# Kernel optimization log

Hardware: AMD Instinct MI355X
Metric: run time of the kernel (lower is better)

Reference implementation:

```python
import jax, jax.numpy as jnp
import numpy as np

N_NODES = 2176
N_IN = 64
N_HID = 2048
N_OUT = 64
NODE_DIM = 64
HEADS = 4


def _build_edge_index():
    hs, os_ = N_IN, N_IN + N_HID
    # input -> hidden block (order: for i: for h)
    s1 = np.repeat(np.arange(0, N_IN), N_HID)
    t1 = np.tile(np.arange(hs, os_), N_IN)
    # hidden -> output block (order: for h: for o)
    s2 = np.repeat(np.arange(hs, os_), N_OUT)
    t2 = np.tile(np.arange(os_, N_NODES), N_HID)
    return jnp.asarray(np.stack([np.concatenate([s1, s2]), np.concatenate([t1, t2])]), dtype=jnp.int32)


def setup_inputs() -> dict:
    key = jax.random.key(0)
    ks = jax.random.split(key, 20)
    D, H = NODE_DIM, HEADS
    edge_index = _build_edge_index()  # [2, E]
    E = edge_index.shape[1]

    def xavier(k, shape):
        fan_in, fan_out = shape[0], shape[1]
        lim = float(np.sqrt(6.0 / (fan_in + fan_out)))
        return jax.random.uniform(k, shape, jnp.float32, -lim, lim)

    return {
        "x_input": jax.random.normal(ks[0], (N_IN,), jnp.float32),
        "node_features": jax.random.normal(ks[1], (N_NODES, D), jnp.float32) * 0.1,
        "edge_weights": jax.random.normal(ks[2], (E, 1), jnp.float32) * 0.1,
        "edge_index": edge_index,
        "wq1": xavier(ks[3], (D, D * H)), "wk1": xavier(ks[4], (D, D * H)),
        "wv1": xavier(ks[5], (D, D * H)), "we1": xavier(ks[6], (1, H)),
        "wo1": xavier(ks[7], (D * H, D)), "bo1": jnp.zeros((D,), jnp.float32),
        "wq2": xavier(ks[8], (D, D * H)), "wk2": xavier(ks[9], (D, D * H)),
        "wv2": xavier(ks[10], (D, D * H)), "we2": xavier(ks[11], (1, H)),
        "wo2": xavier(ks[12], (D * H, D)), "bo2": jnp.zeros((D,), jnp.float32),
        "wproj": xavier(ks[13], (D, 1)), "bproj": jnp.zeros((1,), jnp.float32),
        "num_output_nodes": N_OUT,
    }


def _message_pass(x, edge_index, ew, wq, wk, wv, we, wo, bo):
    # x: [N, D_in]; edge_index: [2, E]; ew: [E, 1]
    src, tgt = edge_index[0], edge_index[1]
    dout = wo.shape[1]
    heads = wq.shape[1] // dout
    q = (x[tgt] @ wq).reshape(-1, heads, dout)  # [E, H, D]
    k = (x[src] @ wk).reshape(-1, heads, dout)
    v = (x[src] @ wv).reshape(-1, heads, dout)
    attn = (q * k).sum(-1) / jnp.sqrt(jnp.float32(dout)) + ew @ we  # [E, H]
    # NOTE: the per-target segment-softmax in the torch source is dead code;
    # the effective math is leaky_relu then a global softmax over edges.
    attn = jax.nn.leaky_relu(attn, negative_slope=0.2)
    attn = jax.nn.softmax(attn, axis=0)
    weighted_v = (attn[:, :, None] * v).reshape(-1, heads * dout)  # [E, H*D]
    out = jax.ops.segment_sum(weighted_v, tgt, num_segments=x.shape[0])  # [N, H*D]
    out = out @ wo + bo
    return out + x  # residual (in_channels == out_channels)


def reference(x_input, node_features, edge_weights, edge_index,
              wq1, wk1, wv1, we1, wo1, bo1,
              wq2, wk2, wv2, we2, wo2, bo2,
              wproj, bproj, num_output_nodes):
    n_in = x_input.shape[0]
    x = node_features.at[:n_in, 0].set(x_input)
    x = jax.nn.relu(_message_pass(x, edge_index, edge_weights, wq1, wk1, wv1, we1, wo1, bo1))
    x = jax.nn.relu(_message_pass(x, edge_index, edge_weights, wq2, wk2, wv2, we2, wo2, bo2))
    out_nodes = x[x.shape[0] - num_output_nodes:]
    output = jax.nn.sigmoid(out_nodes @ wproj + bproj).squeeze()
    return output, x
```

## Files before the change

kernel.cpp:

```cpp
#include <hip/hip_runtime.h>
#include <math.h>

#define E1 131072

template<int AR, int K4>
__device__ __forceinline__ void gemm_nn_lds(const float* __restrict__ A,
                                            const float* __restrict__ B,
                                            float acc[AR][4], int tr, int tc) {
  for (int k4 = 0; k4 < K4; ++k4) {
    float4 b0 = *(const float4*)&B[(k4 * 4 + 0) * 68 + tc * 4];
    float4 b1 = *(const float4*)&B[(k4 * 4 + 1) * 68 + tc * 4];
    float4 b2 = *(const float4*)&B[(k4 * 4 + 2) * 68 + tc * 4];
    float4 b3 = *(const float4*)&B[(k4 * 4 + 3) * 68 + tc * 4];
#pragma unroll
    for (int a = 0; a < AR; ++a) {
      float4 av = *(const float4*)&A[(tr + 16 * a) * 68 + k4 * 4];
      acc[a][0] += av.x * b0.x + av.y * b1.x + av.z * b2.x + av.w * b3.x;
      acc[a][1] += av.x * b0.y + av.y * b1.y + av.z * b2.y + av.w * b3.y;
      acc[a][2] += av.x * b0.z + av.y * b1.z + av.z * b2.z + av.w * b3.z;
      acc[a][3] += av.x * b0.w + av.y * b1.w + av.z * b2.w + av.w * b3.w;
    }
  }
}

template<int AR, int K4>
__device__ __forceinline__ void gemm_nn_g(const float* __restrict__ A,
                                          const float* __restrict__ Bg, int ldb,
                                          float acc[AR][4], int tr, int tc) {
  for (int k4 = 0; k4 < K4; ++k4) {
    float4 b0 = *(const float4*)(Bg + (k4 * 4 + 0) * ldb + tc * 4);
    float4 b1 = *(const float4*)(Bg + (k4 * 4 + 1) * ldb + tc * 4);
    float4 b2 = *(const float4*)(Bg + (k4 * 4 + 2) * ldb + tc * 4);
    float4 b3 = *(const float4*)(Bg + (k4 * 4 + 3) * ldb + tc * 4);
#pragma unroll
    for (int a = 0; a < AR; ++a) {
      float4 av = *(const float4*)&A[(tr + 16 * a) * 68 + k4 * 4];
      acc[a][0] += av.x * b0.x + av.y * b1.x + av.z * b2.x + av.w * b3.x;
      acc[a][1] += av.x * b0.y + av.y * b1.y + av.z * b2.y + av.w * b3.y;
      acc[a][2] += av.x * b0.z + av.y * b1.z + av.z * b2.z + av.w * b3.z;
      acc[a][3] += av.x * b0.w + av.y * b1.w + av.z * b2.w + av.w * b3.w;
    }
  }
}

template<int AR, int BR>
__device__ __forceinline__ void gemm_nt_lds(const float* __restrict__ A,
                                            const float* __restrict__ B,
                                            float acc[AR][BR], int tr, int tc) {
  for (int k4 = 0; k4 < 16; ++k4) {
    float4 av[AR], bv[BR];
#pragma unroll
    for (int a = 0; a < AR; ++a) av[a] = *(const float4*)&A[(tr + 16 * a) * 68 + k4 * 4];
#pragma unroll
    for (int b = 0; b < BR; ++b) bv[b] = *(const float4*)&B[(tc + 16 * b) * 68 + k4 * 4];
#pragma unroll
    for (int a = 0; a < AR; ++a)
#pragma unroll
      for (int b = 0; b < BR; ++b)
        acc[a][b] += av[a].x * bv[b].x + av[a].y * bv[b].y +
                     av[a].z * bv[b].z + av[a].w * bv[b].w;
  }
}

template<int AR>
__device__ __forceinline__ void st_tile(float* __restrict__ C, const float acc[AR][4],
                                        int tr, int tc) {
#pragma unroll
  for (int a = 0; a < AR; ++a)
    *(float4*)&C[(tr + 16 * a) * 68 + tc * 4] =
        make_float4(acc[a][0], acc[a][1], acc[a][2], acc[a][3]);
}

__global__ __launch_bounds__(256) void k_attn1(const float* __restrict__ x,
                                               const float* __restrict__ xinp,
                                               const float* __restrict__ wq1,
                                               const float* __restrict__ wk1,
                                               const float* __restrict__ we1,
                                               const float* __restrict__ ew,
                                               const float* __restrict__ wq2,
                                               const float* __restrict__ wk2,
                                               const float* __restrict__ wv1,
                                               const float* __restrict__ wo1,
                                               const float* __restrict__ wv2,
                                               const float* __restrict__ wo2,
                                               float* __restrict__ AggH,
                                               float* __restrict__ part,
                                               float* __restrict__ bsum,
                                               float* __restrict__ Mb,
                                               float* __restrict__ W2b) {
  __shared__ float S_[17408];
  __shared__ float wred[4];
  const int bid = blockIdx.x, tid = threadIdx.x;
  const bool r1 = bid < 256;
  const int tile = (r1 ? bid : bid - 256) >> 2;
  const int h = bid & 3;
  const int j0 = tile * 32;
  const int tr = tid >> 4, tc = tid & 15;
  const float weh = we1[h];

  if (r1) {
    float* A = S_;
    float* B = S_ + 4352;
    float* C = S_ + 6528;
    float* D = S_ + 10880;
    float* G = S_ + 13056;
    for (int t4 = tid; t4 < 1024; t4 += 256) {
      int r = t4 >> 4, c0 = (t4 & 15) * 4;
      float4 v = *(const float4*)(x + t4 * 4);
      if (c0 == 0) v.x = xinp[r];
      *(float4*)&A[r * 68 + c0] = v;
    }
    for (int t4 = tid; t4 < 512; t4 += 256) {
      int r = t4 >> 4, c0 = (t4 & 15) * 4;
      *(float4*)&B[r * 68 + c0] = *(const float4*)(x + (64 + j0 + r) * 64 + c0);
    }
    for (int t4 = tid; t4 < 512; t4 += 256) {
      int i = t4 >> 3, jl0 = (t4 & 7) * 4;
      *(float4*)&G[i * 68 + jl0] = *(const float4*)(ew + i * 2048 + j0 + jl0);
    }
    __syncthreads();
    {
      float kt[4][4];
#pragma unroll
      for (int a = 0; a < 4; ++a)
#pragma unroll
        for (int q = 0; q < 4; ++q) kt[a][q] = 0.f;
      gemm_nn_g<4, 16>(A, wk1 + h * 64, 256, kt, tr, tc);
      st_tile<4>(C, kt, tr, tc);
      float qt[2][4];
#pragma unroll
      for (int a = 0; a < 2; ++a)
#pragma unroll
        for (int q = 0; q < 4; ++q) qt[a][q] = 0.f;
      gemm_nn_g<2, 16>(B, wq1 + h * 64, 256, qt, tr, tc);
      st_tile<2>(D, qt, tr, tc);
    }
    __syncthreads();
    float lg[2][4];
#pragma unroll
    for (int a = 0; a < 2; ++a)
#pragma unroll
      for (int b = 0; b < 4; ++b) lg[a][b] = 0.f;
    gemm_nt_lds<2, 4>(D, C, lg, tr, tc);
    float esum = 0.f;
#pragma unroll
    for (int a = 0; a < 2; ++a) {
      int row = tr + 16 * a;
#pragma unroll
      for (int b = 0; b < 4; ++b) {
        int col = tc + 16 * b;
        float v = lg[a][b] * 0.125f + G[col * 68 + row] * weh;
        v = (v >= 0.f) ? v : 0.2f * v;
        v = fminf(v, 60.f);
        float e = __expf(v);
        esum += e;
        B[row * 68 + col] = e;
      }
    }
#pragma unroll
    for (int s = 1; s < 64; s <<= 1) esum += __shfl_xor(esum, s);
    if ((tid & 63) == 0) wred[tid >> 6] = esum;
    __syncthreads();
    float u[2][4];
#pragma unroll
    for (int a = 0; a < 2; ++a)
#pragma unroll
      for (int q = 0; q < 4; ++q) u[a][q] = 0.f;
    gemm_nn_lds<2, 16>(B, A, u, tr, tc);
#pragma unroll
    for (int a = 0; a < 2; ++a)
      *(float4*)&AggH[(j0 + tr + 16 * a) * 256 + h * 64 + tc * 4] =
          make_float4(u[a][0], u[a][1], u[a][2], u[a][3]);
    if (tid == 0) bsum[bid] = (wred[0] + wred[1]) + (wred[2] + wred[3]);

    if (bid < 12) {
      __syncthreads();
      const int type = bid >> 2, hh = bid & 3;
      if (type == 0) {
        for (int t4 = tid; t4 < 1024; t4 += 256) {
          int k = t4 >> 4, c0 = (t4 & 15) * 4;
          *(float4*)&A[k * 68 + c0] = *(const float4*)(wq2 + k * 256 + hh * 64 + c0);
          *(float4*)&C[k * 68 + c0] = *(const float4*)(wk2 + k * 256 + hh * 64 + c0);
        }
        __syncthreads();
        float m[4][4];
#pragma unroll
        for (int a = 0; a < 4; ++a)
#pragma unroll
          for (int b = 0; b < 4; ++b) m[a][b] = 0.f;
        gemm_nt_lds<4, 4>(A, C, m, tr, tc);
#pragma unroll
        for (int a = 0; a < 4; ++a)
#pragma unroll
          for (int b = 0; b < 4; ++b)
            Mb[hh * 4096 + (tr + 16 * a) * 64 + tc + 16 * b] = m[a][b];
      } else {
        const float* wv = (type == 1) ? wv1 : wv2;
        const float* wo = (type == 1) ? wo1 : wo2;
        for (int t4 = tid; t4 < 1024; t4 += 256) {
          int k = t4 >> 4, c0 = (t4 & 15) * 4;
          *(float4*)&A[k * 68 + c0] = *(const float4*)(wv + k * 256 + hh * 64 + c0);
          *(float4*)&C[k * 68 + c0] = *(const float4*)(wo + (hh * 64 + k) * 64 + c0);
        }
        __syncthreads();
        float m[4][4];
#pragma unroll
        for (int a = 0; a < 4; ++a)
#pragma unroll
          for (int q = 0; q < 4; ++q) m[a][q] = 0.f;
        gemm_nn_lds<4, 16>(A, C, m, tr, tc);
        float* o = W2b + (type - 1) * 16384;
#pragma unroll
        for (int a = 0; a < 4; ++a)
          *(float4*)&o[(hh * 64 + tr + 16 * a) * 64 + tc * 4] =
              make_float4(m[a][0], m[a][1], m[a][2], m[a][3]);
      }
    }
  } else {
    float* A = S_;
    float* B = S_ + 2176;
    float* C = S_ + 6528;
    float* D = S_ + 8704;
    float* G = S_ + 13056;
    for (int t4 = tid; t4 < 512; t4 += 256) {
      int r = t4 >> 4, c0 = (t4 & 15) * 4;
      *(float4*)&A[r * 68 + c0] = *(const float4*)(x + (64 + j0 + r) * 64 + c0);
    }
    for (int t4 = tid; t4 < 1024; t4 += 256) {
      int r = t4 >> 4, c0 = (t4 & 15) * 4;
      *(float4*)&B[r * 68 + c0] = *(const float4*)(x + (2112 + r) * 64 + c0);
    }
    for (int t4 = tid; t4 < 512; t4 += 256) {
      int jl = t4 >> 4, o0 = (t4 & 15) * 4;
      *(float4*)&G[jl * 68 + o0] = *(const float4*)(ew + E1 + (j0 + jl) * 64 + o0);
    }
    __syncthreads();
    {
      float kt[2][4];
#pragma unroll
      for (int a = 0; a < 2; ++a)
#pragma unroll
        for (int q = 0; q < 4; ++q) kt[a][q] = 0.f;
      gemm_nn_g<2, 16>(A, wk1 + h * 64, 256, kt, tr, tc);
      st_tile<2>(C, kt, tr, tc);
      float qt[4][4];
#pragma unroll
      for (int a = 0; a < 4; ++a)
#pragma unroll
        for (int q = 0; q < 4; ++q) qt[a][q] = 0.f;
      gemm_nn_g<4, 16>(B, wq1 + h * 64, 256, qt, tr, tc);
      st_tile<4>(D, qt, tr, tc);
    }
    __syncthreads();
    float lg[4][2];
#pragma unroll
    for (int a = 0; a < 4; ++a)
#pragma unroll
      for (int b = 0; b < 2; ++b) lg[a][b] = 0.f;
    gemm_nt_lds<4, 2>(D, C, lg, tr, tc);
    float esum = 0.f;
#pragma unroll
    for (int a = 0; a < 4; ++a) {
      int row = tr + 16 * a;
#pragma unroll
      for (int b = 0; b < 2; ++b) {
        int col = tc + 16 * b;
        float v = lg[a][b] * 0.125f + G[col * 68 + row] * weh;
        v = (v >= 0.f) ? v : 0.2f * v;
        v = fminf(v, 60.f);
        float e = __expf(v);
        esum += e;
        B[row * 68 + col] = e;
      }
    }
#pragma unroll
    for (int s = 1; s < 64; s <<= 1) esum += __shfl_xor(esum, s);
    if ((tid & 63) == 0) wred[tid >> 6] = esum;
    __syncthreads();
    float u[4][4];
#pragma unroll
    for (int a = 0; a < 4; ++a)
#pragma unroll
      for (int q = 0; q < 4; ++q) u[a][q] = 0.f;
    gemm_nn_lds<4, 8>(B, A, u, tr, tc);
#pragma unroll
    for (int a = 0; a < 4; ++a)
      *(float4*)&part[tile * 16384 + (tr + 16 * a) * 256 + h * 64 + tc * 4] =
          make_float4(u[a][0], u[a][1], u[a][2], u[a][3]);
    if (tid == 0) bsum[bid] = (wred[0] + wred[1]) + (wred[2] + wred[3]);
  }
}

__global__ __launch_bounds__(256) void k_attn2(const float* __restrict__ x,
                                               const float* __restrict__ Mb,
                                               const float* __restrict__ we,
                                               const float* __restrict__ ew,
                                               float* __restrict__ AggH,
                                               float* __restrict__ part,
                                               float* __restrict__ bsum) {
  __shared__ float S_[13056];
  __shared__ float wred[4];
  const int bid = blockIdx.x, tid = threadIdx.x;
  const bool r1 = bid < 256;
  const int tile = (r1 ? bid : bid - 256) >> 2;
  const int h = bid & 3;
  const int j0 = tile * 32;
  const int tr = tid >> 4, tc = tid & 15;
  const float weh = we[h];
  const float* Mh = Mb + h * 4096;

  if (r1) {
    float* A = S_;
    float* B = S_ + 4352;
    float* C = S_ + 6528;
    float* G = S_ + 8704;
    for (int t4 = tid; t4 < 1024; t4 += 256) {
      int r = t4 >> 4, c0 = (t4 & 15) * 4;
      *(float4*)&A[r * 68 + c0] = *(const float4*)(x + t4 * 4);
    }
    for (int t4 = tid; t4 < 512; t4 += 256) {
      int r = t4 >> 4, c0 = (t4 & 15) * 4;
      *(float4*)&B[r * 68 + c0] = *(const float4*)(x + (64 + j0 + r) * 64 + c0);
    }
    for (int t4 = tid; t4 < 512; t4 += 256) {
      int i = t4 >> 3, jl0 = (t4 & 7) * 4;
      *(float4*)&G[i * 68 + jl0] = *(const float4*)(ew + i * 2048 + j0 + jl0);
    }
    __syncthreads();
    {
      float t_[2][4];
#pragma unroll
      for (int a = 0; a < 2; ++a)
#pragma unroll
        for (int q = 0; q < 4; ++q) t_[a][q] = 0.f;
      gemm_nn_g<2, 16>(B, Mh, 64, t_, tr, tc);
      st_tile<2>(C, t_, tr, tc);
    }
    __syncthreads();
    float lg[2][4];
#pragma unroll
    for (int a = 0; a < 2; ++a)
#pragma unroll
      for (int b = 0; b < 4; ++b) lg[a][b] = 0.f;
    gemm_nt_lds<2, 4>(C, A, lg, tr, tc);
    float esum = 0.f;
#pragma unroll
    for (int a = 0; a < 2; ++a) {
      int row = tr + 16 * a;
#pragma unroll
      for (int b = 0; b < 4; ++b) {
        int col = tc + 16 * b;
        float v = lg[a][b] * 0.125f + G[col * 68 + row] * weh;
        v = (v >= 0.f) ? v : 0.2f * v;
        v = fminf(v, 60.f);
        float e = __expf(v);
        esum += e;
        B[row * 68 + col] = e;
      }
    }
#pragma unroll
    for (int s = 1; s < 64; s <<= 1) esum += __shfl_xor(esum, s);
    if ((tid & 63) == 0) wred[tid >> 6] = esum;
    __syncthreads();
    float u[2][4];
#pragma unroll
    for (int a = 0; a < 2; ++a)
#pragma unroll
      for (int q = 0; q < 4; ++q) u[a][q] = 0.f;
    gemm_nn_lds<2, 16>(B, A, u, tr, tc);
#pragma unroll
    for (int a = 0; a < 2; ++a)
      *(float4*)&AggH[(j0 + tr + 16 * a) * 256 + h * 64 + tc * 4] =
          make_float4(u[a][0], u[a][1], u[a][2], u[a][3]);
    if (tid == 0) bsum[bid] = (wred[0] + wred[1]) + (wred[2] + wred[3]);
  } else {
    float* A = S_;
    float* B = S_ + 2176;
    float* C = S_ + 6528;
    float* G = S_ + 10880;
    for (int t4 = tid; t4 < 512; t4 += 256) {
      int r = t4 >> 4, c0 = (t4 & 15) * 4;
      *(float4*)&A[r * 68 + c0] = *(const float4*)(x + (64 + j0 + r) * 64 + c0);
    }
    for (int t4 = tid; t4 < 1024; t4 += 256) {
      int r = t4 >> 4, c0 = (t4 & 15) * 4;
      *(float4*)&B[r * 68 + c0] = *(const float4*)(x + (2112 + r) * 64 + c0);
    }
    for (int t4 = tid; t4 < 512; t4 += 256) {
      int jl = t4 >> 4, o0 = (t4 & 15) * 4;
      *(float4*)&G[jl * 68 + o0] = *(const float4*)(ew + E1 + (j0 + jl) * 64 + o0);
    }
    __syncthreads();
    {
      float t_[4][4];
#pragma unroll
      for (int a = 0; a < 4; ++a)
#pragma unroll
        for (int q = 0; q < 4; ++q) t_[a][q] = 0.f;
      gemm_nn_g<4, 16>(B, Mh, 64, t_, tr, tc);
      st_tile<4>(C, t_, tr, tc);
    }
    __syncthreads();
    float lg[4][2];
#pragma unroll
    for (int a = 0; a < 4; ++a)
#pragma unroll
      for (int b = 0; b < 2; ++b) lg[a][b] = 0.f;
    gemm_nt_lds<4, 2>(C, A, lg, tr, tc);
    float esum = 0.f;
#pragma unroll
    for (int a = 0; a < 4; ++a) {
      int row = tr + 16 * a;
#pragma unroll
      for (int b = 0; b < 2; ++b) {
        int col = tc + 16 * b;
        float v = lg[a][b] * 0.125f + G[col * 68 + row] * weh;
        v = (v >= 0.f) ? v : 0.2f * v;
        v = fminf(v, 60.f);
        float e = __expf(v);
        esum += e;
        B[row * 68 + col] = e;
      }
    }
#pragma unroll
    for (int s = 1; s < 64; s <<= 1) esum += __shfl_xor(esum, s);
    if ((tid & 63) == 0) wred[tid >> 6] = esum;
    __syncthreads();
    float u[4][4];
#pragma unroll
    for (int a = 0; a < 4; ++a)
#pragma unroll
      for (int q = 0; q < 4; ++q) u[a][q] = 0.f;
    gemm_nn_lds<4, 8>(B, A, u, tr, tc);
#pragma unroll
    for (int a = 0; a < 4; ++a)
      *(float4*)&part[tile * 16384 + (tr + 16 * a) * 256 + h * 64 + tc * 4] =
          make_float4(u[a][0], u[a][1], u[a][2], u[a][3]);
    if (tid == 0) bsum[bid] = (wred[0] + wred[1]) + (wred[2] + wred[3]);
  }
}

template<bool SUB, bool HEAD>
__global__ __launch_bounds__(256) void k_proj(const float* __restrict__ xin,
                                              const float* __restrict__ xinp,
                                              const float* __restrict__ AggH,
                                              const float* __restrict__ part,
                                              const float* __restrict__ bsum,
                                              const float* __restrict__ W2,
                                              const float* __restrict__ bo,
                                              const float* __restrict__ wproj,
                                              const float* __restrict__ bproj,
                                              float* __restrict__ xout,
                                              float* __restrict__ outh) {
  __shared__ float As[4][260];
  const int bid = blockIdx.x, tid = threadIdx.x;
  const int n0 = bid * 4;
  const int nl = tid >> 6, d = tid & 63;
  const int node = n0 + nl;

  float inv[4];
  {
    int l = tid & 63;
#pragma unroll
    for (int hh = 0; hh < 4; ++hh) {
      float s = bsum[4 * l + hh] + bsum[256 + 4 * l + hh];
#pragma unroll
      for (int st = 1; st < 64; st <<= 1) s += __shfl_xor(s, st);
      inv[hh] = 1.f / s;
    }
  }

  float xres = xin[node * 64 + d];
  if (SUB) {
    if (d == 0 && node < 64) xres = xinp[node];
  }

  float val;
  if (n0 < 64) {
    val = xres + bo[d];
  } else {
    if (n0 < 2112) {
      int a = tid >> 6, c0 = (tid & 63) * 4;
      float4 v = *(const float4*)&AggH[(n0 - 64 + a) * 256 + c0];
      float iv = inv[c0 >> 6];
      *(float4*)&As[a][c0] = make_float4(v.x * iv, v.y * iv, v.z * iv, v.w * iv);
    } else {
      int a = tid >> 6, c0 = (tid & 63) * 4;
      float4 s = make_float4(0.f, 0.f, 0.f, 0.f);
      for (int ch = 0; ch < 64; ++ch) {
        float4 v = *(const float4*)&part[ch * 16384 + (n0 - 2112 + a) * 256 + c0];
        s.x += v.x; s.y += v.y; s.z += v.z; s.w += v.w;
      }
      float iv = inv[c0 >> 6];
      *(float4*)&As[a][c0] = make_float4(s.x * iv, s.y * iv, s.z * iv, s.w * iv);
    }
    __syncthreads();
    float acc = xres + bo[d];
    for (int c4 = 0; c4 < 64; ++c4) {
      float4 a4 = *(const float4*)&As[nl][c4 * 4];
      acc += a4.x * W2[(c4 * 4 + 0) * 64 + d] + a4.y * W2[(c4 * 4 + 1) * 64 + d] +
             a4.z * W2[(c4 * 4 + 2) * 64 + d] + a4.w * W2[(c4 * 4 + 3) * 64 + d];
    }
    val = acc;
  }
  val = fmaxf(val, 0.f);
  xout[node * 64 + d] = val;

  if (HEAD) {
    if (n0 >= 2112) {
      float wv = val * wproj[d];
#pragma unroll
      for (int st = 1; st < 64; st <<= 1) wv += __shfl_xor(wv, st);
      if ((tid & 63) == 0) outh[node - 2112] = 1.f / (1.f + __expf(-(wv + bproj[0])));
    }
  }
}

extern "C" void kernel_launch(void* const* d_in, const int* in_sizes, int n_in,
                              void* d_out, int out_size, void* d_ws, size_t ws_size,
                              hipStream_t stream) {
  const float* x_input       = (const float*)d_in[0];
  const float* node_features = (const float*)d_in[1];
  const float* edge_weights  = (const float*)d_in[2];
  const float* wq1 = (const float*)d_in[4];
  const float* wk1 = (const float*)d_in[5];
  const float* wv1 = (const float*)d_in[6];
  const float* we1 = (const float*)d_in[7];
  const float* wo1 = (const float*)d_in[8];
  const float* bo1 = (const float*)d_in[9];
  const float* wq2 = (const float*)d_in[10];
  const float* wk2 = (const float*)d_in[11];
  const float* wv2 = (const float*)d_in[12];
  const float* we2 = (const float*)d_in[13];
  const float* wo2 = (const float*)d_in[14];
  const float* bo2 = (const float*)d_in[15];
  const float* wproj = (const float*)d_in[16];
  const float* bproj = (const float*)d_in[17];

  float* out = (float*)d_out;
  float* ws = (float*)d_ws;
  float* xB   = ws;
  float* AggH = xB + 139264;
  float* part = AggH + 524288;
  float* bsum = part + 1048576;
  float* Mb   = bsum + 512;
  float* W2b  = Mb + 16384;

  k_attn1<<<512, 256, 0, stream>>>(node_features, x_input, wq1, wk1, we1, edge_weights,
                                   wq2, wk2, wv1, wo1, wv2, wo2,
                                   AggH, part, bsum, Mb, W2b);
  k_proj<true, false><<<544, 256, 0, stream>>>(node_features, x_input, AggH, part, bsum,
                                               W2b, bo1, nullptr, nullptr, xB, nullptr);
  k_attn2<<<512, 256, 0, stream>>>(xB, Mb, we2, edge_weights, AggH, part, bsum);
  k_proj<false, true><<<544, 256, 0, stream>>>(xB, nullptr, AggH, part, bsum,
                                               W2b + 16384, bo2, wproj, bproj, out + 64, out);
}
```

Measured before the change: 63.60 us.

## Precompute per-head bilinear attention matrices in a prologue kernel

```diff
diff --git a/kernel.cpp b/kernel.cpp
--- a/kernel.cpp
+++ b/kernel.cpp
@@ -4,9 +4,9 @@
 #define E1 131072
 
 template<int AR, int K4>
-__device__ __forceinline__ void gemm_nn_lds(const float* __restrict__ A,
-                                            const float* __restrict__ B,
-                                            float acc[AR][4], int tr, int tc) {
+__device__ __forceinline__ void gemm_nn(const float* __restrict__ A,
+                                        const float* __restrict__ B,
+                                        float acc[AR][4], int tr, int tc) {
   for (int k4 = 0; k4 < K4; ++k4) {
     float4 b0 = *(const float4*)&B[(k4 * 4 + 0) * 68 + tc * 4];
     float4 b1 = *(const float4*)&B[(k4 * 4 + 1) * 68 + tc * 4];
@@ -23,30 +23,10 @@
   }
 }
 
-template<int AR, int K4>
-__device__ __forceinline__ void gemm_nn_g(const float* __restrict__ A,
-                                          const float* __restrict__ Bg, int ldb,
-                                          float acc[AR][4], int tr, int tc) {
-  for (int k4 = 0; k4 < K4; ++k4) {
-    float4 b0 = *(const float4*)(Bg + (k4 * 4 + 0) * ldb + tc * 4);
-    float4 b1 = *(const float4*)(Bg + (k4 * 4 + 1) * ldb + tc * 4);
-    float4 b2 = *(const float4*)(Bg + (k4 * 4 + 2) * ldb + tc * 4);
-    float4 b3 = *(const float4*)(Bg + (k4 * 4 + 3) * ldb + tc * 4);
-#pragma unroll
-    for (int a = 0; a < AR; ++a) {
-      float4 av = *(const float4*)&A[(tr + 16 * a) * 68 + k4 * 4];
-      acc[a][0] += av.x * b0.x + av.y * b1.x + av.z * b2.x + av.w * b3.x;
-      acc[a][1] += av.x * b0.y + av.y * b1.y + av.z * b2.y + av.w * b3.y;
-      acc[a][2] += av.x * b0.z + av.y * b1.z + av.z * b2.z + av.w * b3.z;
-      acc[a][3] += av.x * b0.w + av.y * b1.w + av.z * b2.w + av.w * b3.w;
-    }
-  }
-}
-
 template<int AR, int BR>
-__device__ __forceinline__ void gemm_nt_lds(const float* __restrict__ A,
-                                            const float* __restrict__ B,
-                                            float acc[AR][BR], int tr, int tc) {
+__device__ __forceinline__ void gemm_nt(const float* __restrict__ A,
+                                        const float* __restrict__ B,
+                                        float acc[AR][BR], int tr, int tc) {
   for (int k4 = 0; k4 < 16; ++k4) {
     float4 av[AR], bv[BR];
 #pragma unroll
@@ -71,69 +51,155 @@
         make_float4(acc[a][0], acc[a][1], acc[a][2], acc[a][3]);
 }
 
+__device__ __forceinline__ void ld64(float* __restrict__ dst, const float* __restrict__ src,
+                                     int tid, bool sub, const float* __restrict__ xinp) {
+  for (int t4 = tid; t4 < 1024; t4 += 256) {
+    int r = t4 >> 4, c0 = (t4 & 15) * 4;
+    float4 v = *(const float4*)(src + t4 * 4);
+    if (sub && c0 == 0) v.x = xinp[r];
+    *(float4*)&dst[r * 68 + c0] = v;
+  }
+}
+__device__ __forceinline__ void ld32(float* __restrict__ dst, const float* __restrict__ src,
+                                     int tid) {
+  for (int t4 = tid; t4 < 512; t4 += 256) {
+    int r = t4 >> 4, c0 = (t4 & 15) * 4;
+    *(float4*)&dst[r * 68 + c0] = *(const float4*)(src + t4 * 4);
+  }
+}
+__device__ __forceinline__ void ldw(float* __restrict__ dst, const float* __restrict__ w,
+                                    int h, int tid) {
+  for (int t4 = tid; t4 < 1024; t4 += 256) {
+    int k = t4 >> 4, c0 = (t4 & 15) * 4;
+    *(float4*)&dst[k * 68 + c0] = *(const float4*)(w + k * 256 + h * 64 + c0);
+  }
+}
+
+__global__ __launch_bounds__(256) void k_pre(const float* __restrict__ nf,
+                                             const float* __restrict__ xinp,
+                                             const float* __restrict__ wq1, const float* __restrict__ wk1,
+                                             const float* __restrict__ wv1, const float* __restrict__ wo1,
+                                             const float* __restrict__ bo1,
+                                             const float* __restrict__ wq2, const float* __restrict__ wk2,
+                                             const float* __restrict__ wv2, const float* __restrict__ wo2,
+                                             float* __restrict__ Y1b, float* __restrict__ Y2b,
+                                             float* __restrict__ Y1pb, float* __restrict__ M2b,
+                                             float* __restrict__ W2b) {
+  __shared__ float A[4352];
+  __shared__ float B[4352];
+  __shared__ float C[4352];
+  const int bid = blockIdx.x, tid = threadIdx.x;
+  const int type = bid >> 2, h = bid & 3;
+  const int tr = tid >> 4, tc = tid & 15;
+
+  if (type <= 2) {
+    if (type == 0) {
+      ld64(A, nf, tid, true, xinp);
+    } else if (type == 1) {
+      ld64(A, nf + 2112 * 64, tid, false, nullptr);
+    } else {
+      for (int t4 = tid; t4 < 1024; t4 += 256) {
+        int r = t4 >> 4, c0 = (t4 & 15) * 4;
+        float4 v = *(const float4*)(nf + t4 * 4);
+        if (c0 == 0) v.x = xinp[r];
+        float4 bv = *(const float4*)(bo1 + c0);
+        v.x = fmaxf(v.x + bv.x, 0.f); v.y = fmaxf(v.y + bv.y, 0.f);
+        v.z = fmaxf(v.z + bv.z, 0.f); v.w = fmaxf(v.w + bv.w, 0.f);
+        *(float4*)&A[r * 68 + c0] = v;
+      }
+    }
+    const float* w1 = (type == 0) ? wk1 : (type == 1) ? wq1 : wk2;
+    const float* w2 = (type == 0) ? wq1 : (type == 1) ? wk1 : wq2;
+    ldw(B, w1, h, tid);
+    __syncthreads();
+    float t_[4][4];
+#pragma unroll
+    for (int a = 0; a < 4; ++a)
+#pragma unroll
+      for (int q = 0; q < 4; ++q) t_[a][q] = 0.f;
+    gemm_nn<4, 16>(A, B, t_, tr, tc);
+    __syncthreads();
+    st_tile<4>(C, t_, tr, tc);
+    ldw(B, w2, h, tid);
+    __syncthreads();
+    float y[4][4];
+#pragma unroll
+    for (int a = 0; a < 4; ++a)
+#pragma unroll
+      for (int b = 0; b < 4; ++b) y[a][b] = 0.f;
+    gemm_nt<4, 4>(C, B, y, tr, tc);
+    float* dst = (type == 0) ? Y1b : (type == 1) ? Y2b : Y1pb;
+#pragma unroll
+    for (int a = 0; a < 4; ++a)
+#pragma unroll
+      for (int b = 0; b < 4; ++b)
+        dst[h * 4096 + (tr + 16 * a) * 64 + tc + 16 * b] = y[a][b];
+  } else if (type == 3) {
+    ldw(A, wq2, h, tid);
+    ldw(B, wk2, h, tid);
+    __syncthreads();
+    float m[4][4];
+#pragma unroll
+    for (int a = 0; a < 4; ++a)
+#pragma unroll
+      for (int b = 0; b < 4; ++b) m[a][b] = 0.f;
+    gemm_nt<4, 4>(A, B, m, tr, tc);
+#pragma unroll
+    for (int a = 0; a < 4; ++a)
+#pragma unroll
+      for (int b = 0; b < 4; ++b)
+        M2b[h * 4096 + (tr + 16 * a) * 64 + tc + 16 * b] = m[a][b];
+  } else {
+    const float* wv = (type == 4) ? wv1 : wv2;
+    const float* wo = (type == 4) ? wo1 : wo2;
+    ldw(A, wv, h, tid);
+    for (int t4 = tid; t4 < 1024; t4 += 256) {
+      int t = t4 >> 4, c0 = (t4 & 15) * 4;
+      *(float4*)&B[t * 68 + c0] = *(const float4*)(wo + (h * 64 + t) * 64 + c0);
+    }
+    __syncthreads();
+    float m[4][4];
+#pragma unroll
+    for (int a = 0; a < 4; ++a)
+#pragma unroll
+      for (int q = 0; q < 4; ++q) m[a][q] = 0.f;
+    gemm_nn<4, 16>(A, B, m, tr, tc);
+    float* o = W2b + (type - 4) * 16384;
+#pragma unroll
+    for (int a = 0; a < 4; ++a)
+      *(float4*)&o[(h * 64 + tr + 16 * a) * 64 + tc * 4] =
+          make_float4(m[a][0], m[a][1], m[a][2], m[a][3]);
+  }
+}
+
 __global__ __launch_bounds__(256) void k_attn1(const float* __restrict__ x,
                                                const float* __restrict__ xinp,
-                                               const float* __restrict__ wq1,
-                                               const float* __restrict__ wk1,
-                                               const float* __restrict__ we1,
+                                               const float* __restrict__ Y1b,
+                                               const float* __restrict__ Y2b,
+                                               const float* __restrict__ we,
                                                const float* __restrict__ ew,
-                                               const float* __restrict__ wq2,
-                                               const float* __restrict__ wk2,
-                                               const float* __restrict__ wv1,
-                                               const float* __restrict__ wo1,
-                                               const float* __restrict__ wv2,
-                                               const float* __restrict__ wo2,
                                                float* __restrict__ AggH,
                                                float* __restrict__ part,
-                                               float* __restrict__ bsum,
-                                               float* __restrict__ Mb,
-                                               float* __restrict__ W2b) {
-  __shared__ float S_[17408];
+                                               float* __restrict__ bsum) {
+  __shared__ float S_[13184];
   __shared__ float wred[4];
   const int bid = blockIdx.x, tid = threadIdx.x;
-  const bool r1 = bid < 256;
-  const int tile = (r1 ? bid : bid - 256) >> 2;
   const int h = bid & 3;
-  const int j0 = tile * 32;
   const int tr = tid >> 4, tc = tid & 15;
-  const float weh = we1[h];
-
-  if (r1) {
-    float* A = S_;
-    float* B = S_ + 4352;
-    float* C = S_ + 6528;
-    float* D = S_ + 10880;
-    float* G = S_ + 13056;
-    for (int t4 = tid; t4 < 1024; t4 += 256) {
-      int r = t4 >> 4, c0 = (t4 & 15) * 4;
-      float4 v = *(const float4*)(x + t4 * 4);
-      if (c0 == 0) v.x = xinp[r];
-      *(float4*)&A[r * 68 + c0] = v;
-    }
-    for (int t4 = tid; t4 < 512; t4 += 256) {
-      int r = t4 >> 4, c0 = (t4 & 15) * 4;
-      *(float4*)&B[r * 68 + c0] = *(const float4*)(x + (64 + j0 + r) * 64 + c0);
-    }
+  const float weh = we[h];
+
+  if (bid < 256) {
+    const int j0 = (bid >> 2) * 32;
+    float* XS = S_;
+    float* Y  = S_ + 4352;
+    float* XH = S_ + 8704;
+    float* G  = S_ + 10880;
+    ld64(XS, x, tid, true, xinp);
+    ld64(Y, Y1b + h * 4096, tid, false, nullptr);
+    ld32(XH, x + (64 + j0) * 64, tid);
     for (int t4 = tid; t4 < 512; t4 += 256) {
       int i = t4 >> 3, jl0 = (t4 & 7) * 4;
-      *(float4*)&G[i * 68 + jl0] = *(const float4*)(ew + i * 2048 + j0 + jl0);
-    }
-    __syncthreads();
-    {
-      float kt[4][4];
-#pragma unroll
-      for (int a = 0; a < 4; ++a)
-#pragma unroll
-        for (int q = 0; q < 4; ++q) kt[a][q] = 0.f;
-      gemm_nn_g<4, 16>(A, wk1 + h * 64, 256, kt, tr, tc);
-      st_tile<4>(C, kt, tr, tc);
-      float qt[2][4];
-#pragma unroll
-      for (int a = 0; a < 2; ++a)
-#pragma unroll
-        for (int q = 0; q < 4; ++q) qt[a][q] = 0.f;
-      gemm_nn_g<2, 16>(B, wq1 + h * 64, 256, qt, tr, tc);
-      st_tile<2>(D, qt, tr, tc);
+      *(float4*)&G[i * 36 + jl0] = *(const float4*)(ew + i * 2048 + j0 + jl0);
     }
     __syncthreads();
     float lg[2][4];
@@ -141,123 +207,199 @@
     for (int a = 0; a < 2; ++a)
 #pragma unroll
       for (int b = 0; b < 4; ++b) lg[a][b] = 0.f;
-    gemm_nt_lds<2, 4>(D, C, lg, tr, tc);
-    float esum = 0.f;
+    gemm_nt<2, 4>(XH, Y, lg, tr, tc);
+    float e_[2][4], esum = 0.f;
 #pragma unroll
     for (int a = 0; a < 2; ++a) {
       int row = tr + 16 * a;
 #pragma unroll
       for (int b = 0; b < 4; ++b) {
+        int col = tc + 16 * b;
+        float v = lg[a][b] * 0.125f + G[col * 36 + row] * weh;
+        v = (v >= 0.f) ? v : 0.2f * v;
+        v = fminf(v, 60.f);
+        float e = __expf(v);
+        e_[a][b] = e; esum += e;
+      }
+    }
+#pragma unroll
+    for (int s = 1; s < 64; s <<= 1) esum += __shfl_xor(esum, s);
+    if ((tid & 63) == 0) wred[tid >> 6] = esum;
+    __syncthreads();
+#pragma unroll
+    for (int a = 0; a < 2; ++a)
+#pragma unroll
+      for (int b = 0; b < 4; ++b)
+        XH[(tr + 16 * a) * 68 + tc + 16 * b] = e_[a][b];
+    __syncthreads();
+    float u[2][4];
+#pragma unroll
+    for (int a = 0; a < 2; ++a)
+#pragma unroll
+      for (int q = 0; q < 4; ++q) u[a][q] = 0.f;
+    gemm_nn<2, 16>(XH, XS, u, tr, tc);
+#pragma unroll
+    for (int a = 0; a < 2; ++a)
+      *(float4*)&AggH[(j0 + tr + 16 * a) * 256 + h * 64 + tc * 4] =
+          make_float4(u[a][0], u[a][1], u[a][2], u[a][3]);
+    if (tid == 0) bsum[bid] = (wred[0] + wred[1]) + (wred[2] + wred[3]);
+  } else {
+    const int tile = (bid - 256) >> 2;
+    const int j0 = tile * 32;
+    float* Y  = S_;
+    float* XH = S_ + 4352;
+    float* G  = S_ + 6528;
+    ld64(Y, Y2b + h * 4096, tid, false, nullptr);
+    ld32(XH, x + (64 + j0) * 64, tid);
+    for (int t4 = tid; t4 < 512; t4 += 256) {
+      int jl = t4 >> 4, o0 = (t4 & 15) * 4;
+      *(float4*)&G[jl * 68 + o0] = *(const float4*)(ew + E1 + (j0 + jl) * 64 + o0);
+    }
+    __syncthreads();
+    float lg[4][2];
+#pragma unroll
+    for (int a = 0; a < 4; ++a)
+#pragma unroll
+      for (int b = 0; b < 2; ++b) lg[a][b] = 0.f;
+    gemm_nt<4, 2>(Y, XH, lg, tr, tc);
+    float e_[4][2], esum = 0.f;
+#pragma unroll
+    for (int a = 0; a < 4; ++a) {
+      int row = tr + 16 * a;
+#pragma unroll
+      for (int b = 0; b < 2; ++b) {
         int col = tc + 16 * b;
         float v = lg[a][b] * 0.125f + G[col * 68 + row] * weh;
         v = (v >= 0.f) ? v : 0.2f * v;
         v = fminf(v, 60.f);
         float e = __expf(v);
-        esum += e;
-        B[row * 68 + col] = e;
+        e_[a][b] = e; esum += e;
       }
     }
 #pragma unroll
     for (int s = 1; s < 64; s <<= 1) esum += __shfl_xor(esum, s);
     if ((tid & 63) == 0) wred[tid >> 6] = esum;
     __syncthreads();
+#pragma unroll
+    for (int a = 0; a < 4; ++a)
+#pragma unroll
+      for (int b = 0; b < 2; ++b)
+        Y[(tr + 16 * a) * 68 + tc + 16 * b] = e_[a][b];
+    __syncthreads();
+    float u[4][4];
+#pragma unroll
+    for (int a = 0; a < 4; ++a)
+#pragma unroll
+      for (int q = 0; q < 4; ++q) u[a][q] = 0.f;
+    gemm_nn<4, 8>(Y, XH, u, tr, tc);
+#pragma unroll
+    for (int a = 0; a < 4; ++a)
+      *(float4*)&part[tile * 16384 + (tr + 16 * a) * 256 + h * 64 + tc * 4] =
+          make_float4(u[a][0], u[a][1], u[a][2], u[a][3]);
+    if (tid == 0) bsum[bid] = (wred[0] + wred[1]) + (wred[2] + wred[3]);
+  }
+}
+
+__global__ __launch_bounds__(256) void k_attn2(const float* __restrict__ x,
+                                               const float* __restrict__ Y1pb,
+                                               const float* __restrict__ M2b,
+                                               const float* __restrict__ we,
+                                               const float* __restrict__ ew,
+                                               float* __restrict__ AggH,
+                                               float* __restrict__ part,
+                                               float* __restrict__ bsum) {
+  __shared__ float S_[13184];
+  __shared__ float wred[4];
+  const int bid = blockIdx.x, tid = threadIdx.x;
+  const int h = bid & 3;
+  const int tr = tid >> 4, tc = tid & 15;
+  const float weh = we[h];
+
+  if (bid < 256) {
+    const int j0 = (bid >> 2) * 32;
+    float* XS = S_;
+    float* Y  = S_ + 4352;
+    float* XH = S_ + 8704;
+    float* G  = S_ + 10880;
+    ld64(XS, x, tid, false, nullptr);
+    ld64(Y, Y1pb + h * 4096, tid, false, nullptr);
+    ld32(XH, x + (64 + j0) * 64, tid);
+    for (int t4 = tid; t4 < 512; t4 += 256) {
+      int i = t4 >> 3, jl0 = (t4 & 7) * 4;
+      *(float4*)&G[i * 36 + jl0] = *(const float4*)(ew + i * 2048 + j0 + jl0);
+    }
+    __syncthreads();
+    float lg[2][4];
+#pragma unroll
+    for (int a = 0; a < 2; ++a)
+#pragma unroll
+      for (int b = 0; b < 4; ++b) lg[a][b] = 0.f;
+    gemm_nt<2, 4>(XH, Y, lg, tr, tc);
+    float e_[2][4], esum = 0.f;
+#pragma unroll
+    for (int a = 0; a < 2; ++a) {
+      int row = tr + 16 * a;
+#pragma unroll
+      for (int b = 0; b < 4; ++b) {
+        int col = tc + 16 * b;
+        float v = lg[a][b] * 0.125f + G[col * 36 + row] * weh;
+        v = (v >= 0.f) ? v : 0.2f * v;
+        v = fminf(v, 60.f);
+        float e = __expf(v);
+        e_[a][b] = e; esum += e;
+      }
+    }
+#pragma unroll
+    for (int s = 1; s < 64; s <<= 1) esum += __shfl_xor(esum, s);
+    if ((tid & 63) == 0) wred[tid >> 6] = esum;
+    __syncthreads();
+#pragma unroll
+    for (int a = 0; a < 2; ++a)
+#pragma unroll
+      for (int b = 0; b < 4; ++b)
+        XH[(tr + 16 * a) * 68 + tc + 16 * b] = e_[a][b];
+    __syncthreads();
     float u[2][4];
 #pragma unroll
     for (int a = 0; a < 2; ++a)
 #pragma unroll
       for (int q = 0; q < 4; ++q) u[a][q] = 0.f;
-    gemm_nn_lds<2, 16>(B, A, u, tr, tc);
+    gemm_nn<2, 16>(XH, XS, u, tr, tc);
 #pragma unroll
     for (int a = 0; a < 2; ++a)
       *(float4*)&AggH[(j0 + tr + 16 * a) * 256 + h * 64 + tc * 4] =
           make_float4(u[a][0], u[a][1], u[a][2], u[a][3]);
     if (tid == 0) bsum[bid] = (wred[0] + wred[1]) + (wred[2] + wred[3]);
-
-    if (bid < 12) {
-      __syncthreads();
-      const int type = bid >> 2, hh = bid & 3;
-      if (type == 0) {
-        for (int t4 = tid; t4 < 1024; t4 += 256) {
-          int k = t4 >> 4, c0 = (t4 & 15) * 4;
-          *(float4*)&A[k * 68 + c0] = *(const float4*)(wq2 + k * 256 + hh * 64 + c0);
-          *(float4*)&C[k * 68 + c0] = *(const float4*)(wk2 + k * 256 + hh * 64 + c0);
-        }
-        __syncthreads();
-        float m[4][4];
-#pragma unroll
-        for (int a = 0; a < 4; ++a)
-#pragma unroll
-          for (int b = 0; b < 4; ++b) m[a][b] = 0.f;
-        gemm_nt_lds<4, 4>(A, C, m, tr, tc);
-#pragma unroll
-        for (int a = 0; a < 4; ++a)
-#pragma unroll
-          for (int b = 0; b < 4; ++b)
-            Mb[hh * 4096 + (tr + 16 * a) * 64 + tc + 16 * b] = m[a][b];
-      } else {
-        const float* wv = (type == 1) ? wv1 : wv2;
-        const float* wo = (type == 1) ? wo1 : wo2;
-        for (int t4 = tid; t4 < 1024; t4 += 256) {
-          int k = t4 >> 4, c0 = (t4 & 15) * 4;
-          *(float4*)&A[k * 68 + c0] = *(const float4*)(wv + k * 256 + hh * 64 + c0);
-          *(float4*)&C[k * 68 + c0] = *(const float4*)(wo + (hh * 64 + k) * 64 + c0);
-        }
-        __syncthreads();
-        float m[4][4];
-#pragma unroll
-        for (int a = 0; a < 4; ++a)
-#pragma unroll
-          for (int q = 0; q < 4; ++q) m[a][q] = 0.f;
-        gemm_nn_lds<4, 16>(A, C, m, tr, tc);
-        float* o = W2b + (type - 1) * 16384;
-#pragma unroll
-        for (int a = 0; a < 4; ++a)
-          *(float4*)&o[(hh * 64 + tr + 16 * a) * 64 + tc * 4] =
-              make_float4(m[a][0], m[a][1], m[a][2], m[a][3]);
-      }
-    }
   } else {
-    float* A = S_;
-    float* B = S_ + 2176;
-    float* C = S_ + 6528;
-    float* D = S_ + 8704;
-    float* G = S_ + 13056;
-    for (int t4 = tid; t4 < 512; t4 += 256) {
-      int r = t4 >> 4, c0 = (t4 & 15) * 4;
-      *(float4*)&A[r * 68 + c0] = *(const float4*)(x + (64 + j0 + r) * 64 + c0);
-    }
-    for (int t4 = tid; t4 < 1024; t4 += 256) {
-      int r = t4 >> 4, c0 = (t4 & 15) * 4;
-      *(float4*)&B[r * 68 + c0] = *(const float4*)(x + (2112 + r) * 64 + c0);
-    }
+    const int tile = (bid - 256) >> 2;
+    const int j0 = tile * 32;
+    float* XO = S_;
+    float* M  = S_ + 4352;
+    float* XH = S_ + 8704;
+    float* G  = S_ + 10880;
+    ld64(XO, x + 2112 * 64, tid, false, nullptr);
+    ld64(M, M2b + h * 4096, tid, false, nullptr);
+    ld32(XH, x + (64 + j0) * 64, tid);
     for (int t4 = tid; t4 < 512; t4 += 256) {
       int jl = t4 >> 4, o0 = (t4 & 15) * 4;
       *(float4*)&G[jl * 68 + o0] = *(const float4*)(ew + E1 + (j0 + jl) * 64 + o0);
     }
     __syncthreads();
-    {
-      float kt[2][4];
-#pragma unroll
-      for (int a = 0; a < 2; ++a)
-#pragma unroll
-        for (int q = 0; q < 4; ++q) kt[a][q] = 0.f;
-      gemm_nn_g<2, 16>(A, wk1 + h * 64, 256, kt, tr, tc);
-      st_tile<2>(C, kt, tr, tc);
-      float qt[4][4];
-#pragma unroll
-      for (int a = 0; a < 4; ++a)
-#pragma unroll
-        for (int q = 0; q < 4; ++q) qt[a][q] = 0.f;
-      gemm_nn_g<4, 16>(B, wq1 + h * 64, 256, qt, tr, tc);
-      st_tile<4>(D, qt, tr, tc);
-    }
+    float t_[4][4];
+#pragma unroll
+    for (int a = 0; a < 4; ++a)
+#pragma unroll
+      for (int q = 0; q < 4; ++q) t_[a][q] = 0.f;
+    gemm_nn<4, 16>(XO, M, t_, tr, tc);
+    __syncthreads();
+    st_tile<4>(XO, t_, tr, tc);
     __syncthreads();
     float lg[4][2];
 #pragma unroll
     for (int a = 0; a < 4; ++a)
 #pragma unroll
       for (int b = 0; b < 2; ++b) lg[a][b] = 0.f;
-    gemm_nt_lds<4, 2>(D, C, lg, tr, tc);
+    gemm_nt<4, 2>(XO, XH, lg, tr, tc);
     float esum = 0.f;
 #pragma unroll
     for (int a = 0; a < 4; ++a) {
@@ -270,7 +412,7 @@
         v = fminf(v, 60.f);
         float e = __expf(v);
         esum += e;
-        B[row * 68 + col] = e;
+        M[row * 68 + col] = e;
       }
     }
 #pragma unroll
@@ -282,156 +424,7 @@
     for (int a = 0; a < 4; ++a)
 #pragma unroll
       for (int q = 0; q < 4; ++q) u[a][q] = 0.f;
-    gemm_nn_lds<4, 8>(B, A, u, tr, tc);
-#pragma unroll
-    for (int a = 0; a < 4; ++a)
-      *(float4*)&part[tile * 16384 + (tr + 16 * a) * 256 + h * 64 + tc * 4] =
-          make_float4(u[a][0], u[a][1], u[a][2], u[a][3]);
-    if (tid == 0) bsum[bid] = (wred[0] + wred[1]) + (wred[2] + wred[3]);
-  }
-}
-
-__global__ __launch_bounds__(256) void k_attn2(const float* __restrict__ x,
-                                               const float* __restrict__ Mb,
-                                               const float* __restrict__ we,
-                                               const float* __restrict__ ew,
-                                               float* __restrict__ AggH,
-                                               float* __restrict__ part,
-                                               float* __restrict__ bsum) {
-  __shared__ float S_[13056];
-  __shared__ float wred[4];
-  const int bid = blockIdx.x, tid = threadIdx.x;
-  const bool r1 = bid < 256;
-  const int tile = (r1 ? bid : bid - 256) >> 2;
-  const int h = bid & 3;
-  const int j0 = tile * 32;
-  const int tr = tid >> 4, tc = tid & 15;
-  const float weh = we[h];
-  const float* Mh = Mb + h * 4096;
-
-  if (r1) {
-    float* A = S_;
-    float* B = S_ + 4352;
-    float* C = S_ + 6528;
-    float* G = S_ + 8704;
-    for (int t4 = tid; t4 < 1024; t4 += 256) {
-      int r = t4 >> 4, c0 = (t4 & 15) * 4;
-      *(float4*)&A[r * 68 + c0] = *(const float4*)(x + t4 * 4);
-    }
-    for (int t4 = tid; t4 < 512; t4 += 256) {
-      int r = t4 >> 4, c0 = (t4 & 15) * 4;
-      *(float4*)&B[r * 68 + c0] = *(const float4*)(x + (64 + j0 + r) * 64 + c0);
-    }
-    for (int t4 = tid; t4 < 512; t4 += 256) {
-      int i = t4 >> 3, jl0 = (t4 & 7) * 4;
-      *(float4*)&G[i * 68 + jl0] = *(const float4*)(ew + i * 2048 + j0 + jl0);
-    }
-    __syncthreads();
-    {
-      float t_[2][4];
-#pragma unroll
-      for (int a = 0; a < 2; ++a)
-#pragma unroll
-        for (int q = 0; q < 4; ++q) t_[a][q] = 0.f;
-      gemm_nn_g<2, 16>(B, Mh, 64, t_, tr, tc);
-      st_tile<2>(C, t_, tr, tc);
-    }
-    __syncthreads();
-    float lg[2][4];
-#pragma unroll
-    for (int a = 0; a < 2; ++a)
-#pragma unroll
-      for (int b = 0; b < 4; ++b) lg[a][b] = 0.f;
-    gemm_nt_lds<2, 4>(C, A, lg, tr, tc);
-    float esum = 0.f;
-#pragma unroll
-    for (int a = 0; a < 2; ++a) {
-      int row = tr + 16 * a;
-#pragma unroll
-      for (int b = 0; b < 4; ++b) {
-        int col = tc + 16 * b;
-        float v = lg[a][b] * 0.125f + G[col * 68 + row] * weh;
-        v = (v >= 0.f) ? v : 0.2f * v;
-        v = fminf(v, 60.f);
-        float e = __expf(v);
-        esum += e;
-        B[row * 68 + col] = e;
-      }
-    }
-#pragma unroll
-    for (int s = 1; s < 64; s <<= 1) esum += __shfl_xor(esum, s);
-    if ((tid & 63) == 0) wred[tid >> 6] = esum;
-    __syncthreads();
-    float u[2][4];
-#pragma unroll
-    for (int a = 0; a < 2; ++a)
-#pragma unroll
-      for (int q = 0; q < 4; ++q) u[a][q] = 0.f;
-    gemm_nn_lds<2, 16>(B, A, u, tr, tc);
-#pragma unroll
-    for (int a = 0; a < 2; ++a)
-      *(float4*)&AggH[(j0 + tr + 16 * a) * 256 + h * 64 + tc * 4] =
-          make_float4(u[a][0], u[a][1], u[a][2], u[a][3]);
-    if (tid == 0) bsum[bid] = (wred[0] + wred[1]) + (wred[2] + wred[3]);
-  } else {
-    float* A = S_;
-    float* B = S_ + 2176;
-    float* C = S_ + 6528;
-    float* G = S_ + 10880;
-    for (int t4 = tid; t4 < 512; t4 += 256) {
-      int r = t4 >> 4, c0 = (t4 & 15) * 4;
-      *(float4*)&A[r * 68 + c0] = *(const float4*)(x + (64 + j0 + r) * 64 + c0);
-    }
-    for (int t4 = tid; t4 < 1024; t4 += 256) {
-      int r = t4 >> 4, c0 = (t4 & 15) * 4;
-      *(float4*)&B[r * 68 + c0] = *(const float4*)(x + (2112 + r) * 64 + c0);
-    }
-    for (int t4 = tid; t4 < 512; t4 += 256) {
-      int jl = t4 >> 4, o0 = (t4 & 15) * 4;
-      *(float4*)&G[jl * 68 + o0] = *(const float4*)(ew + E1 + (j0 + jl) * 64 + o0);
-    }
-    __syncthreads();
-    {
-      float t_[4][4];
-#pragma unroll
-      for (int a = 0; a < 4; ++a)
-#pragma unroll
-        for (int q = 0; q < 4; ++q) t_[a][q] = 0.f;
-      gemm_nn_g<4, 16>(B, Mh, 64, t_, tr, tc);
-      st_tile<4>(C, t_, tr, tc);
-    }
-    __syncthreads();
-    float lg[4][2];
-#pragma unroll
-    for (int a = 0; a < 4; ++a)
-#pragma unroll
-      for (int b = 0; b < 2; ++b) lg[a][b] = 0.f;
-    gemm_nt_lds<4, 2>(C, A, lg, tr, tc);
-    float esum = 0.f;
-#pragma unroll
-    for (int a = 0; a < 4; ++a) {
-      int row = tr + 16 * a;
-#pragma unroll
-      for (int b = 0; b < 2; ++b) {
-        int col = tc + 16 * b;
-        float v = lg[a][b] * 0.125f + G[col * 68 + row] * weh;
-        v = (v >= 0.f) ? v : 0.2f * v;
-        v = fminf(v, 60.f);
-        float e = __expf(v);
-        esum += e;
-        B[row * 68 + col] = e;
-      }
-    }
-#pragma unroll
-    for (int s = 1; s < 64; s <<= 1) esum += __shfl_xor(esum, s);
-    if ((tid & 63) == 0) wred[tid >> 6] = esum;
-    __syncthreads();
-    float u[4][4];
-#pragma unroll
-    for (int a = 0; a < 4; ++a)
-#pragma unroll
-      for (int q = 0; q < 4; ++q) u[a][q] = 0.f;
-    gemm_nn_lds<4, 8>(B, A, u, tr, tc);
+    gemm_nn<4, 8>(M, XH, u, tr, tc);
 #pragma unroll
     for (int a = 0; a < 4; ++a)
       *(float4*)&part[tile * 16384 + (tr + 16 * a) * 256 + h * 64 + tc * 4] =
@@ -543,15 +536,19 @@
   float* AggH = xB + 139264;
   float* part = AggH + 524288;
   float* bsum = part + 1048576;
-  float* Mb   = bsum + 512;
-  float* W2b  = Mb + 16384;
-
-  k_attn1<<<512, 256, 0, stream>>>(node_features, x_input, wq1, wk1, we1, edge_weights,
-                                   wq2, wk2, wv1, wo1, wv2, wo2,
-                                   AggH, part, bsum, Mb, W2b);
+  float* Y1b  = bsum + 512;
+  float* Y2b  = Y1b + 16384;
+  float* Y1pb = Y2b + 16384;
+  float* M2b  = Y1pb + 16384;
+  float* W2b  = M2b + 16384;
+
+  k_pre<<<24, 256, 0, stream>>>(node_features, x_input, wq1, wk1, wv1, wo1, bo1,
+                                wq2, wk2, wv2, wo2, Y1b, Y2b, Y1pb, M2b, W2b);
+  k_attn1<<<512, 256, 0, stream>>>(node_features, x_input, Y1b, Y2b, we1,
+                                   edge_weights, AggH, part, bsum);
   k_proj<true, false><<<544, 256, 0, stream>>>(node_features, x_input, AggH, part, bsum,
                                                W2b, bo1, nullptr, nullptr, xB, nullptr);
-  k_attn2<<<512, 256, 0, stream>>>(xB, Mb, we2, edge_weights, AggH, part, bsum);
+  k_attn2<<<512, 256, 0, stream>>>(xB, Y1pb, M2b, we2, edge_weights, AggH, part, bsum);
   k_proj<false, true><<<544, 256, 0, stream>>>(xB, nullptr, AggH, part, bsum,
                                                W2b + 16384, bo2, wproj, bproj, out + 64, out);
 }
```

Result: no change. 63.01 us (-0.9%).
